# Performance work log

Hardware: AMD Instinct MI355X
Metric: run time of the kernel (lower is better)

## Reference

```python
import jax, jax.numpy as jnp
import numpy as np

DIM = 1024
HEADS = 16
HEAD_DIM = 64
INNER = HEADS * HEAD_DIM  # 1024
B, N = 4, 2048
EPS = 1e-5


def setup_inputs() -> dict:
    key = jax.random.key(0)
    ks = jax.random.split(key, 5)
    x = jax.random.normal(ks[0], (B, N, DIM), dtype=jnp.float32)
    w_qkv = jax.random.normal(ks[1], (DIM, 3 * INNER), dtype=jnp.float32) * (DIM ** -0.5)
    w_out = jax.random.normal(ks[2], (INNER, DIM), dtype=jnp.float32) * (INNER ** -0.5)
    b_out = jax.random.normal(ks[3], (DIM,), dtype=jnp.float32) * 0.01
    ln_gamma = jnp.ones((DIM,), dtype=jnp.float32)
    ln_beta = jnp.zeros((DIM,), dtype=jnp.float32)
    return {"x": x, "w_qkv": w_qkv, "w_out": w_out, "b_out": b_out,
            "ln_gamma": ln_gamma, "ln_beta": ln_beta}


def reference(x, w_qkv, w_out, b_out, ln_gamma, ln_beta):
    scale = HEAD_DIM ** -0.5
    qkv = x @ w_qkv  # [b, n, 3*inner]
    q, k, v = jnp.split(qkv, 3, axis=-1)
    q = q * scale
    # [b, n, h*d] -> [b, h, n, d]
    def to_heads(t):
        b, n, _ = t.shape
        return t.reshape(b, n, HEADS, HEAD_DIM).transpose(0, 2, 1, 3)
    q, k, v = to_heads(q), to_heads(k), to_heads(v)
    scores = jnp.einsum('bhid,bhjd->bhij', q, k)
    attn = jax.nn.softmax(scores, axis=-1)  # max-subtraction (detached) is internal
    out = jnp.einsum('bhij,bhjd->bhid', attn, v)
    out = out.transpose(0, 2, 1, 3).reshape(x.shape[0], x.shape[1], INNER)
    out = out @ w_out + b_out
    # LayerNorm over last dim
    mu = out.mean(axis=-1, keepdims=True)
    var = out.var(axis=-1, keepdims=True)
    out = (out - mu) * jax.lax.rsqrt(var + EPS)
    return out * ln_gamma + ln_beta
```

## Files before the change

kernel.cpp:

```cpp
#include <hip/hip_runtime.h>


typedef __bf16 bf16;
typedef __bf16 bf16x4 __attribute__((ext_vector_type(4)));
typedef __bf16 bf16x8 __attribute__((ext_vector_type(8)));
typedef float f32x4 __attribute__((ext_vector_type(4)));
typedef float f32x16 __attribute__((ext_vector_type(16)));
typedef unsigned int u32x2 __attribute__((ext_vector_type(2)));
typedef unsigned int u32x4 __attribute__((ext_vector_type(4)));

#define QSCALE_LOG2E 0.18033688011112042f

#define GLOAD_LDS16(gp, lp)                                                   \
  __builtin_amdgcn_global_load_lds(                                           \
      (const __attribute__((address_space(1))) unsigned int*)(const void*)(gp), \
      (__attribute__((address_space(3))) unsigned int*)(void*)(lp), 16, 0, 0)

__device__ __forceinline__ float fexp2(float x) {
#if __has_builtin(__builtin_amdgcn_exp2f)
  return __builtin_amdgcn_exp2f(x);
#else
  return __expf(x * 0.6931471805599453f);
#endif
}

__device__ __forceinline__ unsigned pack2t(float lo, float hi) {
  return __builtin_amdgcn_perm(__float_as_uint(hi), __float_as_uint(lo), 0x07060302u);
}

__global__ __launch_bounds__(256) void prep_k(const float* __restrict__ x,
                                              const float* __restrict__ w_qkv,
                                              const float* __restrict__ w_out,
                                              bf16* __restrict__ xbf,
                                              bf16* __restrict__ wqkvT,
                                              bf16* __restrict__ woutT) {
  __shared__ bf16 t[32][36];
  const int bid = blockIdx.x;
  if (bid < 4096) {
    const size_t i = ((size_t)bid * 256 + threadIdx.x) * 8;
    float4 a = *(const float4*)(x + i);
    float4 b = *(const float4*)(x + i + 4);
    bf16x8 o = {(bf16)a.x, (bf16)a.y, (bf16)a.z, (bf16)a.w,
                (bf16)b.x, (bf16)b.y, (bf16)b.z, (bf16)b.w};
    *(bf16x8*)(xbf + i) = o;
    return;
  }
  const float* in;
  bf16* outp;
  int Kd, Nd, n0, k0;
  if (bid < 4096 + 3072) {
    const int idx = bid - 4096;
    in = w_qkv; outp = wqkvT; Kd = 1024; Nd = 3072;
    n0 = (idx % 96) * 32; k0 = (idx / 96) * 32;
  } else {
    const int idx = bid - 7168;
    in = w_out; outp = woutT; Kd = 1024; Nd = 1024;
    n0 = (idx & 31) * 32; k0 = (idx >> 5) * 32;
  }
  const int r = threadIdx.x >> 3, c4 = (threadIdx.x & 7) * 4;
  float4 v = *(const float4*)(in + (size_t)(k0 + r) * Nd + n0 + c4);
  t[c4 + 0][r] = (bf16)v.x; t[c4 + 1][r] = (bf16)v.y;
  t[c4 + 2][r] = (bf16)v.z; t[c4 + 3][r] = (bf16)v.w;
  __syncthreads();
  bf16x4 o = *(const bf16x4*)&t[r][c4];
  *(bf16x4*)(outp + (size_t)(n0 + r) * Kd + k0 + c4) = o;
}

template <bool QKV>
__global__ __launch_bounds__(256) void gemm2(const bf16* __restrict__ A,
                                             const bf16* __restrict__ Bt,
                                             bf16* __restrict__ C,
                                             bf16* __restrict__ Vt) {
  __shared__ bf16 As[128][32];
  __shared__ bf16 Bs[128][32];
  const int tid = threadIdx.x;
  const int l = tid & 63, w = tid >> 6;
  const int g = l >> 4, q = l & 15;
  const int wm = w >> 1, wn = w & 1;
  const int m0 = blockIdx.x * 128, n0 = blockIdx.y * 128;
  const int lr = l >> 2, lc = (l & 3) * 8;

  f32x4 acc[4][4] = {};

  for (int k0 = 0; k0 < 1024; k0 += 32) {
    __syncthreads();
#pragma unroll
    for (int i = 0; i < 2; i++) {
      const int c = w + i * 4;
      GLOAD_LDS16(A + (size_t)(m0 + c * 16 + lr) * 1024 + k0 + lc, &As[c * 16][0]);
      GLOAD_LDS16(Bt + (size_t)(n0 + c * 16 + lr) * 1024 + k0 + lc, &Bs[c * 16][0]);
    }
    __syncthreads();

    bf16x8 af[4], bfr[4];
#pragma unroll
    for (int mi = 0; mi < 4; mi++)
      af[mi] = *(const bf16x8*)&As[wm * 64 + mi * 16 + q][g * 8];
#pragma unroll
    for (int ni = 0; ni < 4; ni++)
      bfr[ni] = *(const bf16x8*)&Bs[wn * 64 + ni * 16 + q][g * 8];
#pragma unroll
    for (int mi = 0; mi < 4; mi++)
#pragma unroll
      for (int ni = 0; ni < 4; ni++)
        acc[mi][ni] = __builtin_amdgcn_mfma_f32_16x16x32_bf16(af[mi], bfr[ni], acc[mi][ni], 0, 0, 0);
  }

  if (QKV && n0 >= 2048) {
#pragma unroll
    for (int mi = 0; mi < 4; mi++)
#pragma unroll
      for (int ni = 0; ni < 4; ni++) {
        const int vcol = n0 - 2048 + wn * 64 + ni * 16 + q;
        const int h = vcol >> 6, d = vcol & 63;
        const int t0 = m0 + wm * 64 + mi * 16 + g * 4;
        const int b = t0 >> 11, n = t0 & 2047;
        bf16x4 o = {(bf16)acc[mi][ni][0], (bf16)acc[mi][ni][1],
                    (bf16)acc[mi][ni][2], (bf16)acc[mi][ni][3]};
        *(bf16x4*)(Vt + ((size_t)(b * 16 + h) * 64 + d) * 2048 + n) = o;
      }
  } else {
    const int ldc = QKV ? 2048 : 1024;
    const float s = (QKV && n0 < 1024) ? QSCALE_LOG2E : 1.0f;
#pragma unroll
    for (int mi = 0; mi < 4; mi++)
#pragma unroll
      for (int ni = 0; ni < 4; ni++) {
        const int col = n0 + wn * 64 + ni * 16 + q;
#pragma unroll
        for (int r = 0; r < 4; r++) {
          const int row = m0 + wm * 64 + mi * 16 + g * 4 + r;
          C[(size_t)row * ldc + col] = (bf16)(acc[mi][ni][r] * s);
        }
      }
  }
}

__global__ __launch_bounds__(256, 3) void attn_k(const bf16* __restrict__ qk,
                                                 const bf16* __restrict__ vt,
                                                 bf16* __restrict__ aout) {
  __shared__ bf16 Ks[3][64][64];
  __shared__ bf16 Vs[3][64][64];
  const int tid = threadIdx.x;
  const int l = tid & 63, w = tid >> 6;
  const int q = l & 31, hi = l >> 5, q7 = q & 7;

  const int flat = blockIdx.x;
  const int logical = (flat & 7) * 128 + (flat >> 3);
  const int qt = logical & 15, bh = logical >> 4;
  const int h = bh & 15, b = bh >> 4;
  const int qbase = qt * 128 + w * 32;

  const bf16* Kg = qk + (size_t)(b * 2048) * 2048 + 1024 + h * 64;
  const bf16* Vg = vt + ((size_t)(b * 16 + h) * 64) * 2048;

  bf16x8 qf[4];
  {
    const bf16* Qr = qk + (size_t)(b * 2048 + qbase + q) * 2048 + h * 64 + hi * 8;
#pragma unroll
    for (int i = 0; i < 4; i++) qf[i] = *(const bf16x8*)(Qr + i * 16);
  }

  const int r0 = tid >> 3, sp0 = ((tid & 7) ^ (r0 & 7)) * 8;
  const int ub = (tid >> 6) << 9;
#define STAGE_KV(buf, kt)                                                       \
  do {                                                                          \
    bf16* kd = &Ks[buf][0][0];                                                  \
    bf16* vd = &Vs[buf][0][0];                                                  \
    GLOAD_LDS16(Kg + (size_t)((kt) + r0) * 2048 + sp0, kd + ub);                \
    GLOAD_LDS16(Vg + (size_t)r0 * 2048 + (kt) + sp0, vd + ub);                  \
    GLOAD_LDS16(Kg + (size_t)((kt) + 32 + r0) * 2048 + sp0, kd + 2048 + ub);    \
    GLOAD_LDS16(Vg + (size_t)(32 + r0) * 2048 + (kt) + sp0, vd + 2048 + ub);    \
  } while (0)

#define QKT(buf, sA, sB)                                                        \
  do {                                                                          \
    const char* Kb_ = (const char*)&Ks[buf][0][0];                              \
    __builtin_amdgcn_s_setprio(1);                                              \
    {                                                                           \
      f32x16 a_ = {};                                                           \
      _Pragma("unroll")                                                         \
      for (int i = 0; i < 4; i++) {                                             \
        bf16x8 kf = *(const bf16x8*)(Kb_ + q * 128 + (((2 * i + hi) ^ q7) << 4));\
        a_ = __builtin_amdgcn_mfma_f32_32x32x16_bf16(kf, qf[i], a_, 0, 0, 0);   \
      }                                                                         \
      sA = a_;                                                                  \
    }                                                                           \
    {                                                                           \
      f32x16 a_ = {};                                                           \
      _Pragma("unroll")                                                         \
      for (int i = 0; i < 4; i++) {                                             \
        bf16x8 kf = *(const bf16x8*)(Kb_ + (32 + q) * 128 +                     \
                                     (((2 * i + hi) ^ q7) << 4));               \
        a_ = __builtin_amdgcn_mfma_f32_32x32x16_bf16(kf, qf[i], a_, 0, 0, 0);   \
      }                                                                         \
      sB = a_;                                                                  \
    }                                                                           \
    __builtin_amdgcn_s_setprio(0);                                              \
  } while (0)

  f32x16 oacc[2] = {};
  float lsA = 0.f, lsB = 0.f;

  STAGE_KV(0, 0);
  STAGE_KV(1, 64);
  asm volatile("s_waitcnt vmcnt(4)" ::: "memory");
  __builtin_amdgcn_sched_barrier(0);
  __builtin_amdgcn_s_barrier();

  f32x16 s0, s1;
  QKT(0, s0, s1);

  int cur = 0;
  for (int kt = 0; kt < 2048; kt += 64) {
    const int nbuf = (cur == 2) ? 0 : cur + 1;
    const int sbuf = (nbuf == 2) ? 0 : nbuf + 1;

    asm volatile("s_waitcnt vmcnt(0)" ::: "memory");
    __builtin_amdgcn_sched_barrier(0);
    __builtin_amdgcn_s_barrier();

    if (kt + 128 < 2048) STAGE_KV(sbuf, kt + 128);

    f32x16 n0v, n1v;
    QKT(nbuf, n0v, n1v);

#pragma unroll
    for (int r = 0; r < 16; r++) { s0[r] = fexp2(s0[r]); lsA += s0[r]; }
#pragma unroll
    for (int r = 0; r < 16; r++) { s1[r] = fexp2(s1[r]); lsB += s1[r]; }

    bf16x8 pfrag[4];
#pragma unroll
    for (int ks = 0; ks < 2; ks++) {
      const unsigned a0 = pack2t(s0[8 * ks + 0], s0[8 * ks + 1]);
      const unsigned a1 = pack2t(s0[8 * ks + 2], s0[8 * ks + 3]);
      const unsigned b0 = pack2t(s0[8 * ks + 4], s0[8 * ks + 5]);
      const unsigned b1 = pack2t(s0[8 * ks + 6], s0[8 * ks + 7]);
      u32x2 w0 = __builtin_amdgcn_permlane32_swap(a0, b0, false, false);
      u32x2 w1 = __builtin_amdgcn_permlane32_swap(a1, b1, false, false);
      u32x4 bw = {w0[0], w1[0], w0[1], w1[1]};
      pfrag[ks] = __builtin_bit_cast(bf16x8, bw);
    }
#pragma unroll
    for (int ks = 0; ks < 2; ks++) {
      const unsigned a0 = pack2t(s1[8 * ks + 0], s1[8 * ks + 1]);
      const unsigned a1 = pack2t(s1[8 * ks + 2], s1[8 * ks + 3]);
      const unsigned b0 = pack2t(s1[8 * ks + 4], s1[8 * ks + 5]);
      const unsigned b1 = pack2t(s1[8 * ks + 6], s1[8 * ks + 7]);
      u32x2 w0 = __builtin_amdgcn_permlane32_swap(a0, b0, false, false);
      u32x2 w1 = __builtin_amdgcn_permlane32_swap(a1, b1, false, false);
      u32x4 bw = {w0[0], w1[0], w0[1], w1[1]};
      pfrag[2 + ks] = __builtin_bit_cast(bf16x8, bw);
    }

    const char* Vb = (const char*)&Vs[cur][0][0];
    __builtin_amdgcn_s_setprio(1);
#pragma unroll
    for (int dblk = 0; dblk < 2; dblk++) {
      bf16x8 vfr[4];
#pragma unroll
      for (int t = 0; t < 4; t++)
        vfr[t] = *(const bf16x8*)(Vb + (dblk * 32 + q) * 128 + (((2 * t + hi) ^ q7) << 4));
#pragma unroll
      for (int t = 0; t < 4; t++)
        oacc[dblk] = __builtin_amdgcn_mfma_f32_32x32x16_bf16(vfr[t], pfrag[t],
                                                             oacc[dblk], 0, 0, 0);
    }
    __builtin_amdgcn_s_setprio(0);

    s0 = n0v; s1 = n1v;
    cur = nbuf;
  }

  float lsum = lsA + lsB;
  {
    u32x2 t2 = __builtin_amdgcn_permlane32_swap(__float_as_uint(lsum),
                                                __float_as_uint(lsum), false, false);
    lsum = __uint_as_float(t2[0]) + __uint_as_float(t2[1]);
  }
  const float inv = 1.f / lsum;
  bf16* orow = aout + (size_t)(b * 2048 + qbase + q) * 1024 + h * 64 + hi * 4;
#pragma unroll
  for (int dblk = 0; dblk < 2; dblk++)
#pragma unroll
    for (int rg = 0; rg < 4; rg++) {
      bf16x4 o = {(bf16)(oacc[dblk][4 * rg + 0] * inv), (bf16)(oacc[dblk][4 * rg + 1] * inv),
                  (bf16)(oacc[dblk][4 * rg + 2] * inv), (bf16)(oacc[dblk][4 * rg + 3] * inv)};
      *(bf16x4*)(orow + dblk * 32 + rg * 8) = o;
    }
#undef QKT
#undef STAGE_KV
}

__global__ __launch_bounds__(256) void ln_k(const bf16* __restrict__ proj,
                                            const float* __restrict__ bo,
                                            const float* __restrict__ gam,
                                            const float* __restrict__ bet,
                                            float* __restrict__ out) {
  const int tid = threadIdx.x;
  const int l = tid & 63, w = tid >> 6;
  const int row = blockIdx.x * 4 + w;
  const int c0 = l * 16;

  bf16x8 p0 = *(const bf16x8*)(proj + (size_t)row * 1024 + c0);
  bf16x8 p1 = *(const bf16x8*)(proj + (size_t)row * 1024 + c0 + 8);
  float v[16];
#pragma unroll
  for (int j = 0; j < 8; j++) { v[j] = (float)p0[j]; v[8 + j] = (float)p1[j]; }
#pragma unroll
  for (int j = 0; j < 4; j++) {
    float4 bv = *(const float4*)(bo + c0 + j * 4);
    v[4 * j + 0] += bv.x; v[4 * j + 1] += bv.y;
    v[4 * j + 2] += bv.z; v[4 * j + 3] += bv.w;
  }
  float s = 0.f, ss = 0.f;
#pragma unroll
  for (int j = 0; j < 16; j++) { s += v[j]; ss += v[j] * v[j]; }
#pragma unroll
  for (int off = 32; off > 0; off >>= 1) {
    s += __shfl_xor(s, off);
    ss += __shfl_xor(ss, off);
  }
  const float mean = s * (1.f / 1024.f);
  const float var = ss * (1.f / 1024.f) - mean * mean;
  const float rs = rsqrtf(var + 1e-5f);
#pragma unroll
  for (int j = 0; j < 4; j++) {
    float4 gv = *(const float4*)(gam + c0 + j * 4);
    float4 btv = *(const float4*)(bet + c0 + j * 4);
    float4 o;
    o.x = (v[4 * j + 0] - mean) * rs * gv.x + btv.x;
    o.y = (v[4 * j + 1] - mean) * rs * gv.y + btv.y;
    o.z = (v[4 * j + 2] - mean) * rs * gv.z + btv.z;
    o.w = (v[4 * j + 3] - mean) * rs * gv.w + btv.w;
    *(float4*)(out + (size_t)row * 1024 + c0 + j * 4) = o;
  }
}

extern "C" void kernel_launch(void* const* d_in, const int* in_sizes, int n_in,
                              void* d_out, int out_size, void* d_ws, size_t ws_size,
                              hipStream_t stream) {
  const float* x      = (const float*)d_in[0];
  const float* w_qkv  = (const float*)d_in[1];
  const float* w_out  = (const float*)d_in[2];
  const float* b_out  = (const float*)d_in[3];
  const float* gamma  = (const float*)d_in[4];
  const float* beta   = (const float*)d_in[5];
  float* out = (float*)d_out;

  char* ws = (char*)d_ws;
  bf16* xbf   = (bf16*)(ws);
  bf16* wqkvT = (bf16*)(ws + 16777216);
  bf16* woutT = (bf16*)(ws + 23068672);
  bf16* qkbuf = (bf16*)(ws + 25165824);
  bf16* vt    = (bf16*)(ws + 58720256);
  bf16* aout  = xbf;
  bf16* proj  = vt;

  dim3 blk(256);
  prep_k<<<8192, blk, 0, stream>>>(x, w_qkv, w_out, xbf, wqkvT, woutT);
  gemm2<true><<<dim3(64, 24), blk, 0, stream>>>(xbf, wqkvT, qkbuf, vt);
  attn_k<<<1024, blk, 0, stream>>>(qkbuf, vt, aout);
  gemm2<false><<<dim3(64, 8), blk, 0, stream>>>(aout, woutT, proj, nullptr);
  ln_k<<<2048, blk, 0, stream>>>(proj, b_out, gamma, beta, out);
}
```

Baseline: 202.5 us.

## Split K/V staging so V uses double buffer, cutting LDS for 4 blocks/CU

The attention kernel's V tile buffer drops from three stages to two. V is now staged only one tile ahead while K stays two tiles ahead, and launch bounds are raised from 3 to 4 blocks per CU. The smaller shared-memory footprint (40KB instead of 48KB per block) is meant to allow higher occupancy to hide latency. The trade-off is a shorter prefetch distance for V, and 4 waves per SIMD may force fewer registers per thread.

```diff
diff --git a/kernel.cpp b/kernel.cpp
--- a/kernel.cpp
+++ b/kernel.cpp
@@ -136,11 +136,11 @@
   }
 }
 
-__global__ __launch_bounds__(256, 3) void attn_k(const bf16* __restrict__ qk,
+__global__ __launch_bounds__(256, 4) void attn_k(const bf16* __restrict__ qk,
                                                  const bf16* __restrict__ vt,
                                                  bf16* __restrict__ aout) {
   __shared__ bf16 Ks[3][64][64];
-  __shared__ bf16 Vs[3][64][64];
+  __shared__ bf16 Vs[2][64][64];
   const int tid = threadIdx.x;
   const int l = tid & 63, w = tid >> 6;
   const int q = l & 31, hi = l >> 5, q7 = q & 7;
@@ -163,13 +163,16 @@
 
   const int r0 = tid >> 3, sp0 = ((tid & 7) ^ (r0 & 7)) * 8;
   const int ub = (tid >> 6) << 9;
-#define STAGE_KV(buf, kt)                                                       \
+#define STAGE_K(buf, kt)                                                        \
   do {                                                                          \
     bf16* kd = &Ks[buf][0][0];                                                  \
+    GLOAD_LDS16(Kg + (size_t)((kt) + r0) * 2048 + sp0, kd + ub);                \
+    GLOAD_LDS16(Kg + (size_t)((kt) + 32 + r0) * 2048 + sp0, kd + 2048 + ub);    \
+  } while (0)
+#define STAGE_V(buf, kt)                                                        \
+  do {                                                                          \
     bf16* vd = &Vs[buf][0][0];                                                  \
-    GLOAD_LDS16(Kg + (size_t)((kt) + r0) * 2048 + sp0, kd + ub);                \
     GLOAD_LDS16(Vg + (size_t)r0 * 2048 + (kt) + sp0, vd + ub);                  \
-    GLOAD_LDS16(Kg + (size_t)((kt) + 32 + r0) * 2048 + sp0, kd + 2048 + ub);    \
     GLOAD_LDS16(Vg + (size_t)(32 + r0) * 2048 + (kt) + sp0, vd + 2048 + ub);    \
   } while (0)
 
@@ -202,28 +205,29 @@
   f32x16 oacc[2] = {};
   float lsA = 0.f, lsB = 0.f;
 
-  STAGE_KV(0, 0);
-  STAGE_KV(1, 64);
-  asm volatile("s_waitcnt vmcnt(4)" ::: "memory");
+  STAGE_K(0, 0);
+  STAGE_V(0, 0);
+  STAGE_K(1, 64);
+  asm volatile("s_waitcnt vmcnt(0)" ::: "memory");
   __builtin_amdgcn_sched_barrier(0);
   __builtin_amdgcn_s_barrier();
 
   f32x16 s0, s1;
   QKT(0, s0, s1);
 
-  int cur = 0;
+  int kq = 1;
+  int ksb = 2;
+  int vcur = 0;
   for (int kt = 0; kt < 2048; kt += 64) {
-    const int nbuf = (cur == 2) ? 0 : cur + 1;
-    const int sbuf = (nbuf == 2) ? 0 : nbuf + 1;
-
     asm volatile("s_waitcnt vmcnt(0)" ::: "memory");
     __builtin_amdgcn_sched_barrier(0);
     __builtin_amdgcn_s_barrier();
 
-    if (kt + 128 < 2048) STAGE_KV(sbuf, kt + 128);
+    if (kt + 128 < 2048) STAGE_K(ksb, kt + 128);
+    if (kt + 64 < 2048) STAGE_V(vcur ^ 1, kt + 64);
 
     f32x16 n0v, n1v;
-    QKT(nbuf, n0v, n1v);
+    QKT(kq, n0v, n1v);
 
 #pragma unroll
     for (int r = 0; r < 16; r++) { s0[r] = fexp2(s0[r]); lsA += s0[r]; }
@@ -254,7 +258,7 @@
       pfrag[2 + ks] = __builtin_bit_cast(bf16x8, bw);
     }
 
-    const char* Vb = (const char*)&Vs[cur][0][0];
+    const char* Vb = (const char*)&Vs[vcur][0][0];
     __builtin_amdgcn_s_setprio(1);
 #pragma unroll
     for (int dblk = 0; dblk < 2; dblk++) {
@@ -270,7 +274,9 @@
     __builtin_amdgcn_s_setprio(0);
 
     s0 = n0v; s1 = n1v;
-    cur = nbuf;
+    kq = (kq == 2) ? 0 : kq + 1;
+    ksb = (ksb == 2) ? 0 : ksb + 1;
+    vcur ^= 1;
   }
 
   float lsum = lsA + lsB;
@@ -290,7 +296,8 @@
       *(bf16x4*)(orow + dblk * 32 + rg * 8) = o;
     }
 #undef QKT
-#undef STAGE_KV
+#undef STAGE_K
+#undef STAGE_V
 }
 
 __global__ __launch_bounds__(256) void ln_k(const bf16* __restrict__ proj,
```

Result: slower. 283.6 us (+40.1%).
